# Kernel optimization log

Hardware: AMD Instinct MI355X
Metric: run time of the kernel (lower is better)

The kernel has to match this reference:

```python
import jax, jax.numpy as jnp
import numpy as np

HIDDEN = 8192
K = 32
DIMS = [512, 768]
BATCH = 16384

def _xavier(key, shape):
    fan_out, fan_in = shape
    limit = np.sqrt(6.0 / (fan_in + fan_out)).astype(np.float32)
    return jax.random.uniform(key, shape, dtype=jnp.float32, minval=-limit, maxval=limit)

def setup_inputs() -> dict:
    key = jax.random.key(0)
    ks = jax.random.split(key, 6)
    return {
        "x0": jax.random.normal(ks[0], (BATCH, DIMS[0]), dtype=jnp.float32),
        "x1": jax.random.normal(ks[1], (BATCH, DIMS[1]), dtype=jnp.float32),
        "pre_bias0": jnp.zeros((DIMS[0],), dtype=jnp.float32),
        "pre_bias1": jnp.zeros((DIMS[1],), dtype=jnp.float32),
        "enc_w0": _xavier(ks[2], (HIDDEN, DIMS[0])),   # nn.Linear(d0, hidden).weight
        "enc_w1": _xavier(ks[3], (HIDDEN, DIMS[1])),
        "dec_w0": _xavier(ks[4], (DIMS[0], HIDDEN)),   # nn.Linear(hidden, d0).weight
        "dec_w1": _xavier(ks[5], (DIMS[1], HIDDEN)),
        "post_bias0": jnp.zeros((DIMS[0],), dtype=jnp.float32),
        "post_bias1": jnp.zeros((DIMS[1],), dtype=jnp.float32),
        "source_idx": 0,
    }

def _topk_sparse(z, k):
    # keep top-k per row, zero the rest (hard TopK activation)
    vals, idx = jax.lax.top_k(z, k)                      # [B, k]
    rows = jnp.arange(z.shape[0])[:, None]               # [B, 1]
    return jnp.zeros_like(z).at[rows, idx].set(vals)

def reference(x0, x1, pre_bias0, pre_bias1, enc_w0, enc_w1,
              dec_w0, dec_w1, post_bias0, post_bias1, source_idx):
    xs = (x0, x1)
    pbs = (pre_bias0, pre_bias1)
    ews = (enc_w0, enc_w1)
    # encode from source model: pre-bias subtract -> linear -> TopK sparsify
    x = xs[source_idx]
    z_dense = (x - pbs[source_idx]) @ ews[source_idx].T   # [B, HIDDEN]
    z = _topk_sparse(z_dense, K)
    # decode to every model's activation space
    rec0 = z @ dec_w0.T + post_bias0                      # [B, d0]
    rec1 = z @ dec_w1.T + post_bias1                      # [B, d1]
    return (z, rec0, rec1)
```

## Files before the change

kernel.cpp:

```cpp
#include <hip/hip_runtime.h>


#define BATCH  16384
#define HIDDEN 8192
#define DIM0   512
#define DIM1   768
#define TOPK   32
#define CAND_MAX 256
#define LIST_CAP 128
#define STAGE_CAP 32
#define CNT_STRIDE 16
#define WIN_LO 36
#define WIN_HI 64

#define KLO_G 0xBECDu
#define KHI_G 0xC020u

typedef __attribute__((ext_vector_type(8))) short bf16x8;
typedef __attribute__((ext_vector_type(8))) unsigned short u16x8;
typedef __attribute__((ext_vector_type(4))) float f32x4;

__device__ __forceinline__ unsigned fkey16(unsigned short h) {
    return (h & 0x8000u) ? (unsigned)((~h) & 0xFFFFu) : (unsigned)(h | 0x8000u);
}
__device__ __forceinline__ unsigned short f2b(float f) {
    unsigned u = __float_as_uint(f);
    unsigned r = (u + 0x7FFFu + ((u >> 16) & 1u)) >> 16;
    return (unsigned short)r;
}
__device__ __forceinline__ float b2f(unsigned short h) {
    return __uint_as_float(((unsigned)h) << 16);
}
__device__ __forceinline__ void load_lds16(const void* g, void* l) {
    __builtin_amdgcn_global_load_lds((const __attribute__((address_space(1))) void*)g,
                                     (__attribute__((address_space(3))) void*)l, 16, 0, 0);
}
__device__ __forceinline__ unsigned fkey32(float f) {
    unsigned u = __float_as_uint(f);
    return (u & 0x80000000u) ? ~u : (u | 0x80000000u);
}

__global__ void zero_cnt(int* __restrict__ cnt)
{
    cnt[blockIdx.x * 256 + threadIdx.x] = 0;
}

template<int SRC>
__device__ __forceinline__ void convert_impl(
    const float* __restrict__ x, const float* __restrict__ pb,
    const float* __restrict__ w,
    unsigned short* __restrict__ xb, unsigned short* __restrict__ wb)
{
    constexpr int D = SRC ? DIM1 : DIM0;
    const int nx4 = BATCH * D / 4;
    const int nw4 = HIDDEN * D / 4;
    for (int i = blockIdx.x * blockDim.x + threadIdx.x; i < nx4 + nw4;
         i += gridDim.x * blockDim.x) {
        if (i < nx4) {
            float4 v = ((const float4*)x)[i];
            const int k = (i * 4) % D;
            v.x -= pb[k]; v.y -= pb[k + 1]; v.z -= pb[k + 2]; v.w -= pb[k + 3];
            ushort4 o; o.x = f2b(v.x); o.y = f2b(v.y); o.z = f2b(v.z); o.w = f2b(v.w);
            ((ushort4*)xb)[i] = o;
        } else {
            const float4 v = ((const float4*)w)[i - nx4];
            ushort4 o; o.x = f2b(v.x); o.y = f2b(v.y); o.z = f2b(v.z); o.w = f2b(v.w);
            ((ushort4*)wb)[i - nx4] = o;
        }
    }
}

__global__ void convert_xw(const float* __restrict__ x0, const float* __restrict__ x1,
                           const float* __restrict__ pb0, const float* __restrict__ pb1,
                           const float* __restrict__ w0, const float* __restrict__ w1,
                           const int* __restrict__ srcp,
                           unsigned short* __restrict__ xb, unsigned short* __restrict__ wb)
{
    if (*srcp == 0) convert_impl<0>(x0, pb0, w0, xb, wb);
    else            convert_impl<1>(x1, pb1, w1, xb, wb);
}

__global__ void transpose_dec_bf16(const float* __restrict__ dec,
                                   unsigned short* __restrict__ decT, int DD)
{
    __shared__ float t[32][33];
    const int hb = blockIdx.x * 32, db = blockIdx.y * 32;
    const int lx = threadIdx.x, ly = threadIdx.y;
#pragma unroll
    for (int s = 0; s < 32; s += 8)
        t[ly + s][lx] = dec[(size_t)(db + ly + s) * HIDDEN + hb + lx];
    __syncthreads();
#pragma unroll
    for (int s = 0; s < 32; s += 8)
        decT[(size_t)(hb + ly + s) * DD + db + lx] = f2b(t[lx][ly + s]);
}

template<int SRC>
__device__ __forceinline__ void gemm_impl(
    const unsigned short* __restrict__ xb, const unsigned short* __restrict__ wb,
    float* __restrict__ z, int* __restrict__ cnt, unsigned short* __restrict__ clist,
    unsigned short* As, unsigned short* Bs)
{
    constexpr int D = SRC ? DIM1 : DIM0;
    constexpr unsigned KTH = SRC ? 0xBF86u : 0xBF5Du;

    const int nwg = gridDim.x;
    int id = blockIdx.x;
    id = (id & 7) * (nwg >> 3) + (id >> 3);
    const int bx = id & 63;
    const int by = id >> 6;
    const int m0 = by * 128, n0 = bx * 128;

    const int tid  = threadIdx.x;
    const int lane = tid & 63;
    const int wid  = tid >> 6;
    const int wr   = wid >> 1;
    const int wc   = wid & 1;
    const int l15  = lane & 15;
    const int g    = lane >> 4;

    f32x4 acc[4][4];
#pragma unroll
    for (int i = 0; i < 4; ++i)
#pragma unroll
        for (int j = 0; j < 4; ++j) acc[i][j] = (f32x4){0.f, 0.f, 0.f, 0.f};

    for (int k0 = 0; k0 < D; k0 += 64) {
#pragma unroll
        for (int q = 0; q < 4; ++q) {
            const int c   = wid * 256 + q * 64 + lane;
            const int row = c >> 3, jb = c & 7;
            const int j   = jb ^ (row & 7);
            load_lds16(xb + (size_t)(m0 + row) * D + k0 + j * 8,
                       As + (size_t)(wid * 256 + q * 64) * 8);
            load_lds16(wb + (size_t)(n0 + row) * D + k0 + j * 8,
                       Bs + (size_t)(wid * 256 + q * 64) * 8);
        }
        __syncthreads();

#pragma unroll
        for (int kk = 0; kk < 2; ++kk) {
            bf16x8 a[4], b[4];
#pragma unroll
            for (int f = 0; f < 4; ++f) {
                const int rA = wr * 64 + f * 16 + l15;
                const int sA = ((kk * 4 + g) ^ (rA & 7)) * 16;
                a[f] = *(const bf16x8*)((const char*)As + rA * 128 + sA);
                const int rB = wc * 64 + f * 16 + l15;
                const int sB = ((kk * 4 + g) ^ (rB & 7)) * 16;
                b[f] = *(const bf16x8*)((const char*)Bs + rB * 128 + sB);
            }
#pragma unroll
            for (int fi = 0; fi < 4; ++fi)
#pragma unroll
                for (int fj = 0; fj < 4; ++fj)
                    acc[fi][fj] = __builtin_amdgcn_mfma_f32_16x16x32_bf16(
                        a[fi], b[fj], acc[fi][fj], 0, 0, 0);
        }
        __syncthreads();
    }

    int*            cnt_local = (int*)As;
    int*            base_sh   = (int*)As + 128;
    unsigned short* staging   = (unsigned short*)((int*)As + 256);

    if (tid < 128) cnt_local[tid] = 0;
    __syncthreads();

#pragma unroll
    for (int fi = 0; fi < 4; ++fi) {
        const int rl0 = wr * 64 + fi * 16 + g * 4;
#pragma unroll
        for (int fj = 0; fj < 4; ++fj) {
            const int col = n0 + wc * 64 + fj * 16 + l15;
#pragma unroll
            for (int r = 0; r < 4; ++r) {
                const unsigned short sb = f2b(acc[fi][fj][r]);
                unsigned short* zs =
                    (unsigned short*)((char*)z + (size_t)(m0 + rl0 + r) * (HIDDEN * 4));
                zs[col] = sb;
                if (fkey16(sb) > KTH) {
                    const int ls = atomicAdd(&cnt_local[rl0 + r], 1);
                    if (ls < STAGE_CAP)
                        staging[(rl0 + r) * STAGE_CAP + ls] = (unsigned short)col;
                }
            }
        }
    }
    __syncthreads();

    if (tid < 128) {
        const int n = cnt_local[tid];
        if (n > 0) {
            const int add = (n > STAGE_CAP) ? 1000 : n;
            base_sh[tid] = atomicAdd(&cnt[(size_t)(m0 + tid) * CNT_STRIDE], add);
        }
    }
    __syncthreads();

    if (tid < 128) {
        const int n = min(cnt_local[tid], STAGE_CAP);
        if (n > 0) {
            const int base = base_sh[tid];
            for (int j = 0; j < n; ++j) {
                const int pos = base + j;
                if (pos < LIST_CAP)
                    clist[(size_t)(m0 + tid) * LIST_CAP + pos] =
                        staging[tid * STAGE_CAP + j];
            }
        }
    }

    if (bx >= 32) {
        const f32x4 zv = (f32x4){0.f, 0.f, 0.f, 0.f};
        const int c4 = (4096 >> 2) + (bx - 32) * 32 + (tid & 31);
#pragma unroll
        for (int pass = 0; pass < 16; ++pass) {
            const int r = m0 + pass * 8 + (tid >> 5);
            __builtin_nontemporal_store(zv, (f32x4*)(z + (size_t)r * HIDDEN) + c4);
        }
    }
}

__global__ __launch_bounds__(256, 2)
void gemm_bf16(const unsigned short* __restrict__ xb, const unsigned short* __restrict__ wb,
               const int* __restrict__ srcp, float* __restrict__ z,
               int* __restrict__ cnt, unsigned short* __restrict__ clist)
{
    __shared__ unsigned short As[128 * 64];
    __shared__ unsigned short Bs[128 * 64];
    if (*srcp == 0) gemm_impl<0>(xb, wb, z, cnt, clist, As, Bs);
    else            gemm_impl<1>(xb, wb, z, cnt, clist, As, Bs);
}

template<int SRC>
__device__ __forceinline__ void topk_impl(
    float* __restrict__ z,
    const float* __restrict__ xsrc, const float* __restrict__ pb,
    const float* __restrict__ ew,
    const unsigned short* __restrict__ dTb0, const unsigned short* __restrict__ dTb1,
    const float* __restrict__ po0, const float* __restrict__ po1,
    float* __restrict__ rec0, float* __restrict__ rec1,
    const int* __restrict__ cnt, const unsigned short* __restrict__ clist,
    float* xs, int* cidx, float* cval, unsigned char* cflag,
    int* counts, unsigned* pcounts, int* s_cnt, float* selv, int* seli)
{
    constexpr int D = SRC ? DIM1 : DIM0;

    const int tid = threadIdx.x;
    const size_t row = blockIdx.x;
    float* __restrict__ zrow = z + row * HIDDEN;
    const unsigned short* __restrict__ zsrow =
        (const unsigned short*)((const char*)z + row * (HIDDEN * 4));

    if (tid < D / 4) {
        const float4 xv = ((const float4*)(xsrc + row * D))[tid];
        const float4 pv = ((const float4*)pb)[tid];
        ((float4*)xs)[tid] = make_float4(xv.x - pv.x, xv.y - pv.y,
                                         xv.z - pv.z, xv.w - pv.w);
    }
    if (tid == 0) *s_cnt = 0;

    const int cn = cnt[row * CNT_STRIDE];
    const bool uselist = (cn >= WIN_LO && cn <= LIST_CAP);
    const f32x4 zv4 = (f32x4){0.f, 0.f, 0.f, 0.f};
    int C;

    if (uselist) {
        if (tid < cn) cidx[tid] = (int)clist[row * LIST_CAP + tid];
#pragma unroll
        for (int s = 0; s < 4; ++s)
            __builtin_nontemporal_store(zv4, (f32x4*)&zrow[(size_t)(s * 256 + tid) * 4]);
        __syncthreads();
        C = cn;
    } else {
        unsigned pkey[16];
#pragma unroll
        for (int s = 0; s < 4; ++s) {
            const u16x8 v = *(const u16x8*)(zsrow + (size_t)(s * 256 + tid) * 8);
#pragma unroll
            for (int p = 0; p < 4; ++p)
                pkey[s * 4 + p] = fkey16(v[2 * p]) | (fkey16(v[2 * p + 1]) << 16);
        }
#pragma unroll
        for (int s = 0; s < 4; ++s)
            __builtin_nontemporal_store(zv4, (f32x4*)&zrow[(size_t)(s * 256 + tid) * 4]);

        {
            int clo = 0, chi = 0;
#pragma unroll
            for (int p = 0; p < 16; ++p) {
                const unsigned klo16 = pkey[p] & 0xFFFFu, khi16 = pkey[p] >> 16;
                clo += (klo16 > KLO_G) ? 1 : 0;  chi += (klo16 > KHI_G) ? 1 : 0;
                clo += (khi16 > KLO_G) ? 1 : 0;  chi += (khi16 > KHI_G) ? 1 : 0;
            }
            unsigned pk = (unsigned)clo | ((unsigned)chi << 16);
#pragma unroll
            for (int off = 32; off; off >>= 1) pk += __shfl_xor(pk, off);
            if ((tid & 63) == 0) pcounts[tid >> 6] = pk;
        }
        __syncthreads();
        const unsigned ptot = pcounts[0] + pcounts[1] + pcounts[2] + pcounts[3];
        const int tot_lo = (int)(ptot & 0xFFFFu), tot_hi = (int)(ptot >> 16);

        unsigned kappa;
        int found = 0;
        if (tot_lo >= WIN_LO && tot_lo <= WIN_HI)      { kappa = KLO_G; found = 1; }
        else if (tot_hi >= WIN_LO && tot_hi <= WIN_HI) { kappa = KHI_G; found = 1; }
        if (!found) {
            unsigned lo = 0u, hi = 65535u;
            if (tot_lo > WIN_HI) lo = KLO_G;
            if (tot_lo < WIN_LO) hi = KLO_G;
            if (tot_hi > WIN_HI) lo = KHI_G;
            if (tot_hi < WIN_LO) hi = (hi < KHI_G) ? hi : KHI_G;
            kappa = lo;
            for (int it = 0; it < 18; ++it) {
                const unsigned mid = (lo + hi) >> 1;
                int c = 0;
#pragma unroll
                for (int p = 0; p < 16; ++p) {
                    c += ((pkey[p] & 0xFFFFu) > mid) ? 1 : 0;
                    c += ((pkey[p] >> 16)     > mid) ? 1 : 0;
                }
#pragma unroll
                for (int off = 32; off; off >>= 1) c += __shfl_xor(c, off);
                if ((tid & 63) == 0) counts[(it & 1) * 4 + (tid >> 6)] = c;
                __syncthreads();
                const int* cb = counts + (it & 1) * 4;
                const int tot = cb[0] + cb[1] + cb[2] + cb[3];
                if (tot >= WIN_LO && tot <= WIN_HI) { kappa = mid; break; }
                if (tot > WIN_HI) lo = mid; else hi = mid;
                kappa = lo;
                if (hi - lo <= 1u) break;
            }
        }

#pragma unroll
        for (int p = 0; p < 16; ++p) {
#pragma unroll
            for (int h = 0; h < 2; ++h) {
                const unsigned k16 = h ? (pkey[p] >> 16) : (pkey[p] & 0xFFFFu);
                if (k16 > kappa) {
                    const int j = 2 * p + h;
                    const int slot = atomicAdd(s_cnt, 1);
                    if (slot < CAND_MAX)
                        cidx[slot] = ((j >> 3) * 256 + tid) * 8 + (j & 7);
                }
            }
        }
        __syncthreads();
        C = min(*s_cnt, CAND_MAX);
    }

    {
        constexpr int NB = D / 64;
        const int grp = tid >> 4, j16 = tid & 15;
        for (int c = grp; c < C; c += 16) {
            const float* __restrict__ wrow = ew + (size_t)cidx[c] * D;
            float4 wv[NB];
#pragma unroll
            for (int u = 0; u < NB; ++u)
                wv[u] = *(const float4*)&wrow[(u * 16 + j16) * 4];
            float4 a4 = make_float4(0.f, 0.f, 0.f, 0.f);
#pragma unroll
            for (int u = 0; u < NB; ++u) {
                const float4 x4 = *(const float4*)&xs[(u * 16 + j16) * 4];
                a4.x = fmaf(x4.x, wv[u].x, a4.x);
                a4.y = fmaf(x4.y, wv[u].y, a4.y);
                a4.z = fmaf(x4.z, wv[u].z, a4.z);
                a4.w = fmaf(x4.w, wv[u].w, a4.w);
            }
            float a = (a4.x + a4.y) + (a4.z + a4.w);
            a += __shfl_xor(a, 1);
            a += __shfl_xor(a, 2);
            a += __shfl_xor(a, 4);
            a += __shfl_xor(a, 8);
            if (j16 == 0) cval[c] = a;
        }
    }
    __syncthreads();

    if (tid < C) {
        const float v = cval[tid];
        const int  ix = cidx[tid];
        int rank = 0;
        for (int j = 0; j < C; ++j) {
            const float vj = cval[j];
            rank += (vj > v || (vj == v && cidx[j] < ix)) ? 1 : 0;
        }
        cflag[tid] = (rank < TOPK) ? 1 : 0;
    }
    __syncthreads();
    if (tid < C && cflag[tid]) {
        const int ix = cidx[tid];
        int sr = 0;
        for (int j = 0; j < C; ++j) sr += (cflag[j] && cidx[j] < ix) ? 1 : 0;
        selv[sr] = cval[tid];
        seli[sr] = ix;
    }
    __syncthreads();

    if (tid < TOPK) zrow[seli[tid]] = selv[tid];

#pragma unroll
    for (int pass = 0; pass < 2; ++pass) {
        const int slot = pass * 256 + tid;
        if (slot < (DIM0 + DIM1) / 4) {
            const bool is0 = slot < DIM0 / 4;
            const int d0 = is0 ? slot * 4 : (slot - DIM0 / 4) * 4;
            const int DD = is0 ? DIM0 : DIM1;
            const unsigned short* __restrict__ dT = is0 ? dTb0 : dTb1;
            const float* __restrict__ po = is0 ? po0 : po1;
            f32x4 a;
            {
                const float4 p4 = *(const float4*)&po[d0];
                a = (f32x4){p4.x, p4.y, p4.z, p4.w};
            }
#pragma unroll
            for (int b = 0; b < TOPK / 16; ++b) {
                ushort4 wv[16];
#pragma unroll
                for (int u = 0; u < 16; ++u)
                    wv[u] = *(const ushort4*)&dT[(size_t)seli[b * 16 + u] * DD + d0];
#pragma unroll
                for (int u = 0; u < 16; ++u) {
                    const float sv = selv[b * 16 + u];
                    a.x = fmaf(sv, b2f(wv[u].x), a.x);
                    a.y = fmaf(sv, b2f(wv[u].y), a.y);
                    a.z = fmaf(sv, b2f(wv[u].z), a.z);
                    a.w = fmaf(sv, b2f(wv[u].w), a.w);
                }
            }
            float* __restrict__ out = is0 ? (rec0 + row * DIM0 + d0)
                                          : (rec1 + row * DIM1 + d0);
            __builtin_nontemporal_store(a, (f32x4*)out);
        }
    }
}

__global__ __launch_bounds__(256, 4)
void topk_rescore_decode(float* __restrict__ z,
                         const float* __restrict__ x0, const float* __restrict__ x1,
                         const float* __restrict__ pb0, const float* __restrict__ pb1,
                         const float* __restrict__ ew0, const float* __restrict__ ew1,
                         const unsigned short* __restrict__ dTb0,
                         const unsigned short* __restrict__ dTb1,
                         const float* __restrict__ po0, const float* __restrict__ po1,
                         float* __restrict__ rec0, float* __restrict__ rec1,
                         const int* __restrict__ srcp,
                         const int* __restrict__ cnt, const unsigned short* __restrict__ clist)
{
    __shared__ float         xs[DIM1];
    __shared__ int           cidx[CAND_MAX];
    __shared__ float         cval[CAND_MAX];
    __shared__ unsigned char cflag[CAND_MAX];
    __shared__ int           counts[2 * 4];
    __shared__ unsigned      pcounts[4];
    __shared__ int           s_cnt;
    __shared__ float         selv[TOPK];
    __shared__ int           seli[TOPK];

    if (*srcp == 0)
        topk_impl<0>(z, x0, pb0, ew0, dTb0, dTb1, po0, po1, rec0, rec1, cnt, clist,
                     xs, cidx, cval, cflag, counts, pcounts, &s_cnt, selv, seli);
    else
        topk_impl<1>(z, x1, pb1, ew1, dTb0, dTb1, po0, po1, rec0, rec1, cnt, clist,
                     xs, cidx, cval, cflag, counts, pcounts, &s_cnt, selv, seli);
}


__global__ __launch_bounds__(256, 2)
void encode_gemm(const float* __restrict__ x0, const float* __restrict__ x1,
                 const float* __restrict__ pb0, const float* __restrict__ pb1,
                 const float* __restrict__ w0, const float* __restrict__ w1,
                 const int* __restrict__ srcp, float* __restrict__ z)
{
    const int src = *srcp;
    const float* __restrict__ x  = (src == 0) ? x0 : x1;
    const float* __restrict__ pb = (src == 0) ? pb0 : pb1;
    const float* __restrict__ w  = (src == 0) ? w0 : w1;
    const int D = (src == 0) ? DIM0 : DIM1;

    __shared__ float As[16][132];
    __shared__ float Bs[16][132];

    const int tid = threadIdx.x;
    const int m0 = blockIdx.y * 128;
    const int n0 = blockIdx.x * 128;

    const int cA0 = tid,          cA1 = tid + 256;
    const int r0  = cA0 >> 2,     kq0 = (cA0 & 3) * 4;
    const int r1  = cA1 >> 2,     kq1 = (cA1 & 3) * 4;

    const int mf = (tid & 15) * 4;
    const int nf = (tid >> 4) * 4;

    float acc[8][8];
#pragma unroll
    for (int i = 0; i < 8; ++i)
#pragma unroll
        for (int j = 0; j < 8; ++j) acc[i][j] = 0.0f;

    for (int k0 = 0; k0 < D; k0 += 16) {
        const float4 av0 = *(const float4*)(x + (size_t)(m0 + r0) * D + k0 + kq0);
        const float4 av1 = *(const float4*)(x + (size_t)(m0 + r1) * D + k0 + kq1);
        const float4 pv0 = *(const float4*)(pb + k0 + kq0);
        const float4 pv1 = *(const float4*)(pb + k0 + kq1);
        const float4 bv0 = *(const float4*)(w + (size_t)(n0 + r0) * D + k0 + kq0);
        const float4 bv1 = *(const float4*)(w + (size_t)(n0 + r1) * D + k0 + kq1);
        As[kq0 + 0][r0] = av0.x - pv0.x;
        As[kq0 + 1][r0] = av0.y - pv0.y;
        As[kq0 + 2][r0] = av0.z - pv0.z;
        As[kq0 + 3][r0] = av0.w - pv0.w;
        As[kq1 + 0][r1] = av1.x - pv1.x;
        As[kq1 + 1][r1] = av1.y - pv1.y;
        As[kq1 + 2][r1] = av1.z - pv1.z;
        As[kq1 + 3][r1] = av1.w - pv1.w;
        Bs[kq0 + 0][r0] = bv0.x;
        Bs[kq0 + 1][r0] = bv0.y;
        Bs[kq0 + 2][r0] = bv0.z;
        Bs[kq0 + 3][r0] = bv0.w;
        Bs[kq1 + 0][r1] = bv1.x;
        Bs[kq1 + 1][r1] = bv1.y;
        Bs[kq1 + 2][r1] = bv1.z;
        Bs[kq1 + 3][r1] = bv1.w;
        __syncthreads();
#pragma unroll
        for (int kk = 0; kk < 16; ++kk) {
            const float4 A0 = *(const float4*)&As[kk][mf];
            const float4 A1 = *(const float4*)&As[kk][mf + 64];
            const float4 B0 = *(const float4*)&Bs[kk][nf];
            const float4 B1 = *(const float4*)&Bs[kk][nf + 64];
            const float a[8] = {A0.x, A0.y, A0.z, A0.w, A1.x, A1.y, A1.z, A1.w};
            const float b[8] = {B0.x, B0.y, B0.z, B0.w, B1.x, B1.y, B1.z, B1.w};
#pragma unroll
            for (int i = 0; i < 8; ++i)
#pragma unroll
                for (int j = 0; j < 8; ++j)
                    acc[i][j] = fmaf(a[i], b[j], acc[i][j]);
        }
        __syncthreads();
    }

#pragma unroll
    for (int i = 0; i < 8; ++i) {
        const int row = m0 + mf + (i & 3) + (i >> 2) * 64;
        const float4 v0 = make_float4(acc[i][0], acc[i][1], acc[i][2], acc[i][3]);
        const float4 v1 = make_float4(acc[i][4], acc[i][5], acc[i][6], acc[i][7]);
        *(float4*)(z + (size_t)row * HIDDEN + n0 + nf)      = v0;
        *(float4*)(z + (size_t)row * HIDDEN + n0 + nf + 64) = v1;
    }
}

__global__ __launch_bounds__(256, 2)
void topk_decode_fb(float* __restrict__ z,
                    const float* __restrict__ dA, const float* __restrict__ dB,
                    const float* __restrict__ po0, const float* __restrict__ po1,
                    float* __restrict__ rec0, float* __restrict__ rec1)
{
    __shared__ float    rowv[HIDDEN];
    __shared__ unsigned hist[4][257];
    __shared__ unsigned scanbuf[256];
    __shared__ float    selv[TOPK];
    __shared__ int      seli[TOPK];
    __shared__ unsigned sh_byte, sh_gt;

    const int tid = threadIdx.x;
    const size_t rowid = blockIdx.x;
    float* __restrict__ zrow = z + rowid * HIDDEN;

#pragma unroll
    for (int s = 0; s < 8; ++s) {
        const int i4 = s * 256 + tid;
        *(float4*)&rowv[i4 * 4] = *(const float4*)&zrow[i4 * 4];
    }
    __syncthreads();

    unsigned prefix = 0, prefmask = 0, need = TOPK;
#pragma unroll
    for (int p = 3; p >= 0; --p) {
        for (int i = tid; i < 4 * 257; i += 256) (&hist[0][0])[i] = 0;
        __syncthreads();
        const int sh = p * 8;
        for (int s = 0; s < 32; ++s) {
            const int i = s * 256 + tid;
            const unsigned k = fkey32(rowv[i]);
            if ((k & prefmask) == prefix)
                atomicAdd(&hist[tid & 3][(k >> sh) & 255], 1);
        }
        __syncthreads();
        const unsigned tot = hist[0][tid] + hist[1][tid] + hist[2][tid] + hist[3][tid];
        hist[0][tid] = tot;
        __syncthreads();
        if (tid == 0) {
            unsigned cum = 0;
            int b = 255;
            for (;; --b) {
                const unsigned c = hist[0][b];
                if (cum + c >= need || b == 0) { sh_byte = (unsigned)b; sh_gt = cum; break; }
                cum += c;
            }
        }
        __syncthreads();
        prefix  |= sh_byte << sh;
        prefmask |= 0xFFu << sh;
        need -= sh_gt;
        __syncthreads();
    }
    const unsigned cut = prefix;
    const unsigned needEq = need;

    unsigned gtmask = 0, eqmask = 0;
#pragma unroll
    for (int j = 0; j < 32; ++j) {
        const int jr = (j + tid) & 31;
        const int i = tid * 32 + jr;
        const unsigned k = fkey32(rowv[i]);
        if (k > cut)       gtmask |= 1u << jr;
        else if (k == cut) eqmask |= 1u << jr;
    }

    scanbuf[tid] = __popc(eqmask);
    __syncthreads();
    for (int off = 1; off < 256; off <<= 1) {
        const unsigned v = scanbuf[tid];
        const unsigned add = (tid >= off) ? scanbuf[tid - off] : 0u;
        __syncthreads();
        scanbuf[tid] = v + add;
        __syncthreads();
    }
    const unsigned eqexc = scanbuf[tid] - __popc(eqmask);
    __syncthreads();

    unsigned selmask = gtmask;
    {
        unsigned m = eqmask, r = eqexc;
        while (m) {
            const int j = __ffs(m) - 1;
            if (r < needEq) selmask |= 1u << j;
            ++r;
            m &= m - 1;
        }
    }

    scanbuf[tid] = __popc(selmask);
    __syncthreads();
    for (int off = 1; off < 256; off <<= 1) {
        const unsigned v = scanbuf[tid];
        const unsigned add = (tid >= off) ? scanbuf[tid - off] : 0u;
        __syncthreads();
        scanbuf[tid] = v + add;
        __syncthreads();
    }
    const unsigned selexc = scanbuf[tid] - __popc(selmask);

#pragma unroll
    for (int j = 0; j < 32; ++j) {
        const int jr = (j + tid) & 31;
        const int i = tid * 32 + jr;
        if ((selmask >> jr) & 1u) {
            const int slot = (int)(selexc + __popc(selmask & ((1u << jr) - 1u)));
            selv[slot] = rowv[i];
            seli[slot] = i;
        } else {
            rowv[i] = 0.0f;
        }
    }
    __syncthreads();

#pragma unroll
    for (int s = 0; s < 8; ++s) {
        const int i4 = s * 256 + tid;
        *(float4*)&zrow[i4 * 4] = *(float4*)&rowv[i4 * 4];
    }

    for (int d = tid; d < DIM0; d += 256) {
        float a = po0[d];
#pragma unroll
        for (int j = 0; j < TOPK; ++j)
            a = fmaf(selv[j], dA[(size_t)d * HIDDEN + seli[j]], a);
        rec0[rowid * DIM0 + d] = a;
    }
    for (int d = tid; d < DIM1; d += 256) {
        float a = po1[d];
#pragma unroll
        for (int j = 0; j < TOPK; ++j)
            a = fmaf(selv[j], dB[(size_t)d * HIDDEN + seli[j]], a);
        rec1[rowid * DIM1 + d] = a;
    }
}

extern "C" void kernel_launch(void* const* d_in, const int* in_sizes, int n_in,
                              void* d_out, int out_size, void* d_ws, size_t ws_size,
                              hipStream_t stream)
{
    const float* x0  = (const float*)d_in[0];
    const float* x1  = (const float*)d_in[1];
    const float* pb0 = (const float*)d_in[2];
    const float* pb1 = (const float*)d_in[3];
    const float* ew0 = (const float*)d_in[4];
    const float* ew1 = (const float*)d_in[5];
    const float* dw0 = (const float*)d_in[6];
    const float* dw1 = (const float*)d_in[7];
    const float* po0 = (const float*)d_in[8];
    const float* po1 = (const float*)d_in[9];
    const int*  srcp = (const int*)d_in[10];

    float* z    = (float*)d_out;
    float* rec0 = z + (size_t)BATCH * HIDDEN;
    float* rec1 = rec0 + (size_t)BATCH * DIM0;

    unsigned short* xb   = (unsigned short*)d_ws;
    unsigned short* wb   = xb   + (size_t)BATCH * DIM1;
    unsigned short* dTb0 = wb   + (size_t)HIDDEN * DIM1;
    unsigned short* dTb1 = dTb0 + (size_t)HIDDEN * DIM0;
    int*            cnt  = (int*)(dTb1 + (size_t)HIDDEN * DIM1);
    unsigned short* clist = (unsigned short*)(cnt + (size_t)BATCH * CNT_STRIDE);
    const size_t need = ((size_t)BATCH * DIM1 + (size_t)HIDDEN * DIM1 +
                         (size_t)HIDDEN * DIM0 + (size_t)HIDDEN * DIM1) * sizeof(unsigned short)
                        + (size_t)BATCH * CNT_STRIDE * sizeof(int)
                        + (size_t)BATCH * LIST_CAP * sizeof(unsigned short);

    if (ws_size >= need) {
        zero_cnt<<<(BATCH * CNT_STRIDE) / 256, 256, 0, stream>>>(cnt);
        convert_xw<<<4096, 256, 0, stream>>>(x0, x1, pb0, pb1, ew0, ew1, srcp, xb, wb);
        dim3 tb(32, 8);
        transpose_dec_bf16<<<dim3(HIDDEN / 32, DIM0 / 32), tb, 0, stream>>>(dw0, dTb0, DIM0);
        transpose_dec_bf16<<<dim3(HIDDEN / 32, DIM1 / 32), tb, 0, stream>>>(dw1, dTb1, DIM1);
        gemm_bf16<<<(BATCH / 128) * (HIDDEN / 128), 256, 0, stream>>>(
            xb, wb, srcp, z, cnt, clist);
        topk_rescore_decode<<<BATCH, 256, 0, stream>>>(
            z, x0, x1, pb0, pb1, ew0, ew1, dTb0, dTb1, po0, po1, rec0, rec1,
            srcp, cnt, clist);
    } else {
        encode_gemm<<<dim3(HIDDEN / 128, BATCH / 128), 256, 0, stream>>>(
            x0, x1, pb0, pb1, ew0, ew1, srcp, z);
        topk_decode_fb<<<BATCH, 256, 0, stream>>>(z, dw0, dw1, po0, po1, rec0, rec1);
    }
}
```

Baseline: 688.5 us.

## Drop bf16 z staging, rescore only top candidates, add exact fallback kernel

The GEMM epilogue no longer writes bf16 scores into z. It now zeros the whole z tile and stages candidate entries as packed (key, column) words chosen by a float threshold. The top-k kernel ranks list candidates and rescores only the best 40 in fp32, and returns early for rows whose candidate count falls outside the window. A new fixup kernel recomputes the full fp32 row with a radix select for those rows. This removes bf16 z traffic and the per-row histogram/bisection path, at the cost of an extra launch and a slow scalar path for outlier rows. It also risks missing true top-k elements when fewer than 40 rescored candidates hold them.

```diff
diff --git a/kernel.cpp b/kernel.cpp
--- a/kernel.cpp
+++ b/kernel.cpp
@@ -6,18 +6,13 @@
 #define DIM0   512
 #define DIM1   768
 #define TOPK   32
-#define CAND_MAX 256
 #define LIST_CAP 128
+#define RESCORE_TOP 40
 #define STAGE_CAP 32
 #define CNT_STRIDE 16
 #define WIN_LO 36
-#define WIN_HI 64
-
-#define KLO_G 0xBECDu
-#define KHI_G 0xC020u
 
 typedef __attribute__((ext_vector_type(8))) short bf16x8;
-typedef __attribute__((ext_vector_type(8))) unsigned short u16x8;
 typedef __attribute__((ext_vector_type(4))) float f32x4;
 
 __device__ __forceinline__ unsigned fkey16(unsigned short h) {
@@ -98,11 +93,11 @@
 template<int SRC>
 __device__ __forceinline__ void gemm_impl(
     const unsigned short* __restrict__ xb, const unsigned short* __restrict__ wb,
-    float* __restrict__ z, int* __restrict__ cnt, unsigned short* __restrict__ clist,
+    float* __restrict__ z, int* __restrict__ cnt, unsigned* __restrict__ clist,
     unsigned short* As, unsigned short* Bs)
 {
     constexpr int D = SRC ? DIM1 : DIM0;
-    constexpr unsigned KTH = SRC ? 0xBF86u : 0xBF5Du;
+    constexpr float THETA = SRC ? 0.96761f : 0.80161f;
 
     const int nwg = gridDim.x;
     int id = blockIdx.x;
@@ -160,9 +155,9 @@
         __syncthreads();
     }
 
-    int*            cnt_local = (int*)As;
-    int*            base_sh   = (int*)As + 128;
-    unsigned short* staging   = (unsigned short*)((int*)As + 256);
+    unsigned* staging   = (unsigned*)As;
+    int*      cnt_local = (int*)Bs;
+    int*      base_sh   = (int*)Bs + 128;
 
     if (tid < 128) cnt_local[tid] = 0;
     __syncthreads();
@@ -175,14 +170,12 @@
             const int col = n0 + wc * 64 + fj * 16 + l15;
 #pragma unroll
             for (int r = 0; r < 4; ++r) {
-                const unsigned short sb = f2b(acc[fi][fj][r]);
-                unsigned short* zs =
-                    (unsigned short*)((char*)z + (size_t)(m0 + rl0 + r) * (HIDDEN * 4));
-                zs[col] = sb;
-                if (fkey16(sb) > KTH) {
+                const float v = acc[fi][fj][r];
+                if (v > THETA) {
                     const int ls = atomicAdd(&cnt_local[rl0 + r], 1);
                     if (ls < STAGE_CAP)
-                        staging[(rl0 + r) * STAGE_CAP + ls] = (unsigned short)col;
+                        staging[(rl0 + r) * STAGE_CAP + ls] =
+                            (fkey16(f2b(v)) << 16) | (0xFFFFu - (unsigned)col);
                 }
             }
         }
@@ -211,9 +204,9 @@
         }
     }
 
-    if (bx >= 32) {
+    {
         const f32x4 zv = (f32x4){0.f, 0.f, 0.f, 0.f};
-        const int c4 = (4096 >> 2) + (bx - 32) * 32 + (tid & 31);
+        const int c4 = bx * 32 + (tid & 31);
 #pragma unroll
         for (int pass = 0; pass < 16; ++pass) {
             const int r = m0 + pass * 8 + (tid >> 5);
@@ -225,7 +218,7 @@
 __global__ __launch_bounds__(256, 2)
 void gemm_bf16(const unsigned short* __restrict__ xb, const unsigned short* __restrict__ wb,
                const int* __restrict__ srcp, float* __restrict__ z,
-               int* __restrict__ cnt, unsigned short* __restrict__ clist)
+               int* __restrict__ cnt, unsigned* __restrict__ clist)
 {
     __shared__ unsigned short As[128 * 64];
     __shared__ unsigned short Bs[128 * 64];
@@ -241,17 +234,18 @@
     const unsigned short* __restrict__ dTb0, const unsigned short* __restrict__ dTb1,
     const float* __restrict__ po0, const float* __restrict__ po1,
     float* __restrict__ rec0, float* __restrict__ rec1,
-    const int* __restrict__ cnt, const unsigned short* __restrict__ clist,
-    float* xs, int* cidx, float* cval, unsigned char* cflag,
-    int* counts, unsigned* pcounts, int* s_cnt, float* selv, int* seli)
+    const int* __restrict__ cnt, const unsigned* __restrict__ clist,
+    float* xs, unsigned* centry, int* cidx, float* cval, unsigned char* cflag,
+    float* selv, int* seli)
 {
     constexpr int D = SRC ? DIM1 : DIM0;
 
     const int tid = threadIdx.x;
     const size_t row = blockIdx.x;
     float* __restrict__ zrow = z + row * HIDDEN;
-    const unsigned short* __restrict__ zsrow =
-        (const unsigned short*)((const char*)z + row * (HIDDEN * 4));
+
+    const int cn = cnt[row * CNT_STRIDE];
+    if (cn < WIN_LO || cn > LIST_CAP) return;
 
     if (tid < D / 4) {
         const float4 xv = ((const float4*)(xsrc + row * D))[tid];
@@ -259,98 +253,17 @@
         ((float4*)xs)[tid] = make_float4(xv.x - pv.x, xv.y - pv.y,
                                          xv.z - pv.z, xv.w - pv.w);
     }
-    if (tid == 0) *s_cnt = 0;
-
-    const int cn = cnt[row * CNT_STRIDE];
-    const bool uselist = (cn >= WIN_LO && cn <= LIST_CAP);
-    const f32x4 zv4 = (f32x4){0.f, 0.f, 0.f, 0.f};
-    int C;
-
-    if (uselist) {
-        if (tid < cn) cidx[tid] = (int)clist[row * LIST_CAP + tid];
-#pragma unroll
-        for (int s = 0; s < 4; ++s)
-            __builtin_nontemporal_store(zv4, (f32x4*)&zrow[(size_t)(s * 256 + tid) * 4]);
-        __syncthreads();
-        C = cn;
-    } else {
-        unsigned pkey[16];
-#pragma unroll
-        for (int s = 0; s < 4; ++s) {
-            const u16x8 v = *(const u16x8*)(zsrow + (size_t)(s * 256 + tid) * 8);
-#pragma unroll
-            for (int p = 0; p < 4; ++p)
-                pkey[s * 4 + p] = fkey16(v[2 * p]) | (fkey16(v[2 * p + 1]) << 16);
-        }
-#pragma unroll
-        for (int s = 0; s < 4; ++s)
-            __builtin_nontemporal_store(zv4, (f32x4*)&zrow[(size_t)(s * 256 + tid) * 4]);
-
-        {
-            int clo = 0, chi = 0;
-#pragma unroll
-            for (int p = 0; p < 16; ++p) {
-                const unsigned klo16 = pkey[p] & 0xFFFFu, khi16 = pkey[p] >> 16;
-                clo += (klo16 > KLO_G) ? 1 : 0;  chi += (klo16 > KHI_G) ? 1 : 0;
-                clo += (khi16 > KLO_G) ? 1 : 0;  chi += (khi16 > KHI_G) ? 1 : 0;
-            }
-            unsigned pk = (unsigned)clo | ((unsigned)chi << 16);
-#pragma unroll
-            for (int off = 32; off; off >>= 1) pk += __shfl_xor(pk, off);
-            if ((tid & 63) == 0) pcounts[tid >> 6] = pk;
-        }
-        __syncthreads();
-        const unsigned ptot = pcounts[0] + pcounts[1] + pcounts[2] + pcounts[3];
-        const int tot_lo = (int)(ptot & 0xFFFFu), tot_hi = (int)(ptot >> 16);
-
-        unsigned kappa;
-        int found = 0;
-        if (tot_lo >= WIN_LO && tot_lo <= WIN_HI)      { kappa = KLO_G; found = 1; }
-        else if (tot_hi >= WIN_LO && tot_hi <= WIN_HI) { kappa = KHI_G; found = 1; }
-        if (!found) {
-            unsigned lo = 0u, hi = 65535u;
-            if (tot_lo > WIN_HI) lo = KLO_G;
-            if (tot_lo < WIN_LO) hi = KLO_G;
-            if (tot_hi > WIN_HI) lo = KHI_G;
-            if (tot_hi < WIN_LO) hi = (hi < KHI_G) ? hi : KHI_G;
-            kappa = lo;
-            for (int it = 0; it < 18; ++it) {
-                const unsigned mid = (lo + hi) >> 1;
-                int c = 0;
-#pragma unroll
-                for (int p = 0; p < 16; ++p) {
-                    c += ((pkey[p] & 0xFFFFu) > mid) ? 1 : 0;
-                    c += ((pkey[p] >> 16)     > mid) ? 1 : 0;
-                }
-#pragma unroll
-                for (int off = 32; off; off >>= 1) c += __shfl_xor(c, off);
-                if ((tid & 63) == 0) counts[(it & 1) * 4 + (tid >> 6)] = c;
-                __syncthreads();
-                const int* cb = counts + (it & 1) * 4;
-                const int tot = cb[0] + cb[1] + cb[2] + cb[3];
-                if (tot >= WIN_LO && tot <= WIN_HI) { kappa = mid; break; }
-                if (tot > WIN_HI) lo = mid; else hi = mid;
-                kappa = lo;
-                if (hi - lo <= 1u) break;
-            }
-        }
-
-#pragma unroll
-        for (int p = 0; p < 16; ++p) {
-#pragma unroll
-            for (int h = 0; h < 2; ++h) {
-                const unsigned k16 = h ? (pkey[p] >> 16) : (pkey[p] & 0xFFFFu);
-                if (k16 > kappa) {
-                    const int j = 2 * p + h;
-                    const int slot = atomicAdd(s_cnt, 1);
-                    if (slot < CAND_MAX)
-                        cidx[slot] = ((j >> 3) * 256 + tid) * 8 + (j & 7);
-                }
-            }
-        }
-        __syncthreads();
-        C = min(*s_cnt, CAND_MAX);
-    }
+    if (tid < cn) centry[tid] = clist[row * LIST_CAP + tid];
+    __syncthreads();
+
+    const int C = min(cn, RESCORE_TOP);
+    if (tid < cn) {
+        const unsigned e = centry[tid];
+        int rank = 0;
+        for (int j = 0; j < cn; ++j) rank += (centry[j] > e) ? 1 : 0;
+        if (rank < RESCORE_TOP) cidx[rank] = (int)(0xFFFFu - (e & 0xFFFFu));
+    }
+    __syncthreads();
 
     {
         constexpr int NB = D / 64;
@@ -448,24 +361,220 @@
                          const float* __restrict__ po0, const float* __restrict__ po1,
                          float* __restrict__ rec0, float* __restrict__ rec1,
                          const int* __restrict__ srcp,
-                         const int* __restrict__ cnt, const unsigned short* __restrict__ clist)
+                         const int* __restrict__ cnt, const unsigned* __restrict__ clist)
 {
     __shared__ float         xs[DIM1];
-    __shared__ int           cidx[CAND_MAX];
-    __shared__ float         cval[CAND_MAX];
-    __shared__ unsigned char cflag[CAND_MAX];
-    __shared__ int           counts[2 * 4];
-    __shared__ unsigned      pcounts[4];
-    __shared__ int           s_cnt;
+    __shared__ unsigned      centry[LIST_CAP];
+    __shared__ int           cidx[RESCORE_TOP];
+    __shared__ float         cval[RESCORE_TOP];
+    __shared__ unsigned char cflag[RESCORE_TOP];
     __shared__ float         selv[TOPK];
     __shared__ int           seli[TOPK];
 
     if (*srcp == 0)
         topk_impl<0>(z, x0, pb0, ew0, dTb0, dTb1, po0, po1, rec0, rec1, cnt, clist,
-                     xs, cidx, cval, cflag, counts, pcounts, &s_cnt, selv, seli);
+                     xs, centry, cidx, cval, cflag, selv, seli);
     else
         topk_impl<1>(z, x1, pb1, ew1, dTb0, dTb1, po0, po1, rec0, rec1, cnt, clist,
-                     xs, cidx, cval, cflag, counts, pcounts, &s_cnt, selv, seli);
+                     xs, centry, cidx, cval, cflag, selv, seli);
+}
+
+template<int SRC>
+__device__ __forceinline__ void fixup_impl(
+    float* __restrict__ z,
+    const float* __restrict__ xsrc, const float* __restrict__ pb,
+    const float* __restrict__ ew,
+    const unsigned short* __restrict__ dTb0, const unsigned short* __restrict__ dTb1,
+    const float* __restrict__ po0, const float* __restrict__ po1,
+    float* __restrict__ rec0, float* __restrict__ rec1,
+    float* sc, float* xs, unsigned* hist, unsigned* scanbuf,
+    float* selv, int* seli, unsigned* sh2)
+{
+    constexpr int D = SRC ? DIM1 : DIM0;
+    const int tid = threadIdx.x;
+    const size_t row = blockIdx.x;
+    float* __restrict__ zrow = z + row * HIDDEN;
+
+    if (tid < D / 4) {
+        const float4 xv = ((const float4*)(xsrc + row * D))[tid];
+        const float4 pv = ((const float4*)pb)[tid];
+        ((float4*)xs)[tid] = make_float4(xv.x - pv.x, xv.y - pv.y,
+                                         xv.z - pv.z, xv.w - pv.w);
+    }
+    __syncthreads();
+
+    for (int s = 0; s < 32; ++s) {
+        const int c = s * 256 + tid;
+        const float* __restrict__ wrow = ew + (size_t)c * D;
+        float a = 0.0f;
+        for (int k = 0; k < D; k += 4) {
+            const float4 w4 = *(const float4*)&wrow[k];
+            a = fmaf(xs[k + 0], w4.x, a);
+            a = fmaf(xs[k + 1], w4.y, a);
+            a = fmaf(xs[k + 2], w4.z, a);
+            a = fmaf(xs[k + 3], w4.w, a);
+        }
+        sc[c] = a;
+    }
+    __syncthreads();
+
+    unsigned prefix = 0, prefmask = 0, need = TOPK;
+#pragma unroll
+    for (int p = 3; p >= 0; --p) {
+        for (int i = tid; i < 4 * 257; i += 256) hist[i] = 0;
+        __syncthreads();
+        const int sh = p * 8;
+        for (int s = 0; s < 32; ++s) {
+            const int i = s * 256 + tid;
+            const unsigned k = fkey32(sc[i]);
+            if ((k & prefmask) == prefix)
+                atomicAdd(&hist[(tid & 3) * 257 + ((k >> sh) & 255)], 1);
+        }
+        __syncthreads();
+        const unsigned tot = hist[0 * 257 + tid] + hist[1 * 257 + tid] +
+                             hist[2 * 257 + tid] + hist[3 * 257 + tid];
+        hist[tid] = tot;
+        __syncthreads();
+        if (tid == 0) {
+            unsigned cum = 0;
+            int b = 255;
+            for (;; --b) {
+                const unsigned c = hist[b];
+                if (cum + c >= need || b == 0) { sh2[0] = (unsigned)b; sh2[1] = cum; break; }
+                cum += c;
+            }
+        }
+        __syncthreads();
+        prefix  |= sh2[0] << sh;
+        prefmask |= 0xFFu << sh;
+        need -= sh2[1];
+        __syncthreads();
+    }
+    const unsigned cut = prefix;
+    const unsigned needEq = need;
+
+    unsigned gtmask = 0, eqmask = 0;
+#pragma unroll
+    for (int j = 0; j < 32; ++j) {
+        const int jr = (j + tid) & 31;
+        const int i = tid * 32 + jr;
+        const unsigned k = fkey32(sc[i]);
+        if (k > cut)       gtmask |= 1u << jr;
+        else if (k == cut) eqmask |= 1u << jr;
+    }
+
+    scanbuf[tid] = __popc(eqmask);
+    __syncthreads();
+    for (int off = 1; off < 256; off <<= 1) {
+        const unsigned v = scanbuf[tid];
+        const unsigned add = (tid >= off) ? scanbuf[tid - off] : 0u;
+        __syncthreads();
+        scanbuf[tid] = v + add;
+        __syncthreads();
+    }
+    const unsigned eqexc = scanbuf[tid] - __popc(eqmask);
+    __syncthreads();
+
+    unsigned selmask = gtmask;
+    {
+        unsigned m = eqmask, r = eqexc;
+        while (m) {
+            const int j = __ffs(m) - 1;
+            if (r < needEq) selmask |= 1u << j;
+            ++r;
+            m &= m - 1;
+        }
+    }
+
+    scanbuf[tid] = __popc(selmask);
+    __syncthreads();
+    for (int off = 1; off < 256; off <<= 1) {
+        const unsigned v = scanbuf[tid];
+        const unsigned add = (tid >= off) ? scanbuf[tid - off] : 0u;
+        __syncthreads();
+        scanbuf[tid] = v + add;
+        __syncthreads();
+    }
+    const unsigned selexc = scanbuf[tid] - __popc(selmask);
+
+#pragma unroll
+    for (int j = 0; j < 32; ++j) {
+        const int jr = (j + tid) & 31;
+        const int i = tid * 32 + jr;
+        if ((selmask >> jr) & 1u) {
+            const int slot = (int)(selexc + __popc(selmask & ((1u << jr) - 1u)));
+            selv[slot] = sc[i];
+            seli[slot] = i;
+        }
+    }
+    __syncthreads();
+
+    if (tid < TOPK) zrow[seli[tid]] = selv[tid];
+
+#pragma unroll
+    for (int pass = 0; pass < 2; ++pass) {
+        const int slot = pass * 256 + tid;
+        if (slot < (DIM0 + DIM1) / 4) {
+            const bool is0 = slot < DIM0 / 4;
+            const int d0 = is0 ? slot * 4 : (slot - DIM0 / 4) * 4;
+            const int DD = is0 ? DIM0 : DIM1;
+            const unsigned short* __restrict__ dT = is0 ? dTb0 : dTb1;
+            const float* __restrict__ po = is0 ? po0 : po1;
+            f32x4 a;
+            {
+                const float4 p4 = *(const float4*)&po[d0];
+                a = (f32x4){p4.x, p4.y, p4.z, p4.w};
+            }
+#pragma unroll
+            for (int b = 0; b < TOPK / 16; ++b) {
+                ushort4 wv[16];
+#pragma unroll
+                for (int u = 0; u < 16; ++u)
+                    wv[u] = *(const ushort4*)&dT[(size_t)seli[b * 16 + u] * DD + d0];
+#pragma unroll
+                for (int u = 0; u < 16; ++u) {
+                    const float sv = selv[b * 16 + u];
+                    a.x = fmaf(sv, b2f(wv[u].x), a.x);
+                    a.y = fmaf(sv, b2f(wv[u].y), a.y);
+                    a.z = fmaf(sv, b2f(wv[u].z), a.z);
+                    a.w = fmaf(sv, b2f(wv[u].w), a.w);
+                }
+            }
+            float* __restrict__ out = is0 ? (rec0 + row * DIM0 + d0)
+                                          : (rec1 + row * DIM1 + d0);
+            __builtin_nontemporal_store(a, (f32x4*)out);
+        }
+    }
+}
+
+__global__ __launch_bounds__(256)
+void fixup_topk(float* __restrict__ z,
+                const float* __restrict__ x0, const float* __restrict__ x1,
+                const float* __restrict__ pb0, const float* __restrict__ pb1,
+                const float* __restrict__ ew0, const float* __restrict__ ew1,
+                const unsigned short* __restrict__ dTb0,
+                const unsigned short* __restrict__ dTb1,
+                const float* __restrict__ po0, const float* __restrict__ po1,
+                float* __restrict__ rec0, float* __restrict__ rec1,
+                const int* __restrict__ srcp, const int* __restrict__ cnt)
+{
+    const int cn = cnt[(size_t)blockIdx.x * CNT_STRIDE];
+    if (cn >= WIN_LO && cn <= LIST_CAP) return;
+
+    __shared__ float    sc[HIDDEN];
+    __shared__ float    xs[DIM1];
+    __shared__ unsigned hist[4 * 257];
+    __shared__ unsigned scanbuf[256];
+    __shared__ float    selv[TOPK];
+    __shared__ int      seli[TOPK];
+    __shared__ unsigned sh2[2];
+
+    if (*srcp == 0)
+        fixup_impl<0>(z, x0, pb0, ew0, dTb0, dTb1, po0, po1, rec0, rec1,
+                      sc, xs, hist, scanbuf, selv, seli, sh2);
+    else
+        fixup_impl<1>(z, x1, pb1, ew1, dTb0, dTb1, po0, po1, rec0, rec1,
+                      sc, xs, hist, scanbuf, selv, seli, sh2);
 }
 
 
@@ -715,11 +824,11 @@
     unsigned short* dTb0 = wb   + (size_t)HIDDEN * DIM1;
     unsigned short* dTb1 = dTb0 + (size_t)HIDDEN * DIM0;
     int*            cnt  = (int*)(dTb1 + (size_t)HIDDEN * DIM1);
-    unsigned short* clist = (unsigned short*)(cnt + (size_t)BATCH * CNT_STRIDE);
+    unsigned*       clist = (unsigned*)(cnt + (size_t)BATCH * CNT_STRIDE);
     const size_t need = ((size_t)BATCH * DIM1 + (size_t)HIDDEN * DIM1 +
                          (size_t)HIDDEN * DIM0 + (size_t)HIDDEN * DIM1) * sizeof(unsigned short)
                         + (size_t)BATCH * CNT_STRIDE * sizeof(int)
-                        + (size_t)BATCH * LIST_CAP * sizeof(unsigned short);
+                        + (size_t)BATCH * LIST_CAP * sizeof(unsigned);
 
     if (ws_size >= need) {
         zero_cnt<<<(BATCH * CNT_STRIDE) / 256, 256, 0, stream>>>(cnt);
@@ -732,6 +841,9 @@
         topk_rescore_decode<<<BATCH, 256, 0, stream>>>(
             z, x0, x1, pb0, pb1, ew0, ew1, dTb0, dTb1, po0, po1, rec0, rec1,
             srcp, cnt, clist);
+        fixup_topk<<<BATCH, 256, 0, stream>>>(
+            z, x0, x1, pb0, pb1, ew0, ew1, dTb0, dTb1, po0, po1, rec0, rec1,
+            srcp, cnt);
     } else {
         encode_gemm<<<dim3(HIDDEN / 128, BATCH / 128), 256, 0, stream>>>(
             x0, x1, pb0, pb1, ew0, ew1, srcp, z);
```

Measured after the change: 1.533 ms. 2.23x slower.

## Rank bf16 candidates and rescore only the top 40 in fp32

Applied to the files above, without the earlier changes.

Candidate entries now pack the bf16 sort key with the column index, both in the GEMM staging list and in the top-k kernel's fallback path. The top-k kernel ranks the candidates by that key and rescores only the best RESCORE_TOP=40 in exact fp32, instead of all of them (up to 128 or 256). This is meant to cut the per-row fp32 recompute work. In exchange the candidate list doubles in size (32-bit entries), a quadratic rank pass is added, and results can be wrong if a true top-32 element ranks below 40th under bf16 rounding.

```diff
diff --git a/kernel.cpp b/kernel.cpp
--- a/kernel.cpp
+++ b/kernel.cpp
@@ -8,6 +8,7 @@
 #define TOPK   32
 #define CAND_MAX 256
 #define LIST_CAP 128
+#define RESCORE_TOP 40
 #define STAGE_CAP 32
 #define CNT_STRIDE 16
 #define WIN_LO 36
@@ -98,7 +99,7 @@
 template<int SRC>
 __device__ __forceinline__ void gemm_impl(
     const unsigned short* __restrict__ xb, const unsigned short* __restrict__ wb,
-    float* __restrict__ z, int* __restrict__ cnt, unsigned short* __restrict__ clist,
+    float* __restrict__ z, int* __restrict__ cnt, unsigned* __restrict__ clist,
     unsigned short* As, unsigned short* Bs)
 {
     constexpr int D = SRC ? DIM1 : DIM0;
@@ -160,9 +161,9 @@
         __syncthreads();
     }
 
-    int*            cnt_local = (int*)As;
-    int*            base_sh   = (int*)As + 128;
-    unsigned short* staging   = (unsigned short*)((int*)As + 256);
+    unsigned* staging   = (unsigned*)As;
+    int*      cnt_local = (int*)Bs;
+    int*      base_sh   = (int*)Bs + 128;
 
     if (tid < 128) cnt_local[tid] = 0;
     __syncthreads();
@@ -179,10 +180,12 @@
                 unsigned short* zs =
                     (unsigned short*)((char*)z + (size_t)(m0 + rl0 + r) * (HIDDEN * 4));
                 zs[col] = sb;
-                if (fkey16(sb) > KTH) {
+                const unsigned k16 = fkey16(sb);
+                if (k16 > KTH) {
                     const int ls = atomicAdd(&cnt_local[rl0 + r], 1);
                     if (ls < STAGE_CAP)
-                        staging[(rl0 + r) * STAGE_CAP + ls] = (unsigned short)col;
+                        staging[(rl0 + r) * STAGE_CAP + ls] =
+                            (k16 << 16) | (unsigned)(8191 - col);
                 }
             }
         }
@@ -225,7 +228,7 @@
 __global__ __launch_bounds__(256, 2)
 void gemm_bf16(const unsigned short* __restrict__ xb, const unsigned short* __restrict__ wb,
                const int* __restrict__ srcp, float* __restrict__ z,
-               int* __restrict__ cnt, unsigned short* __restrict__ clist)
+               int* __restrict__ cnt, unsigned* __restrict__ clist)
 {
     __shared__ unsigned short As[128 * 64];
     __shared__ unsigned short Bs[128 * 64];
@@ -241,8 +244,8 @@
     const unsigned short* __restrict__ dTb0, const unsigned short* __restrict__ dTb1,
     const float* __restrict__ po0, const float* __restrict__ po1,
     float* __restrict__ rec0, float* __restrict__ rec1,
-    const int* __restrict__ cnt, const unsigned short* __restrict__ clist,
-    float* xs, int* cidx, float* cval, unsigned char* cflag,
+    const int* __restrict__ cnt, const unsigned* __restrict__ clist,
+    float* xs, unsigned* centry, int* cidx, float* cval, unsigned char* cflag,
     int* counts, unsigned* pcounts, int* s_cnt, float* selv, int* seli)
 {
     constexpr int D = SRC ? DIM1 : DIM0;
@@ -264,15 +267,15 @@
     const int cn = cnt[row * CNT_STRIDE];
     const bool uselist = (cn >= WIN_LO && cn <= LIST_CAP);
     const f32x4 zv4 = (f32x4){0.f, 0.f, 0.f, 0.f};
-    int C;
+    int cnC;
 
     if (uselist) {
-        if (tid < cn) cidx[tid] = (int)clist[row * LIST_CAP + tid];
+        if (tid < cn) centry[tid] = clist[row * LIST_CAP + tid];
 #pragma unroll
         for (int s = 0; s < 4; ++s)
             __builtin_nontemporal_store(zv4, (f32x4*)&zrow[(size_t)(s * 256 + tid) * 4]);
         __syncthreads();
-        C = cn;
+        cnC = cn;
     } else {
         unsigned pkey[16];
 #pragma unroll
@@ -343,14 +346,25 @@
                 if (k16 > kappa) {
                     const int j = 2 * p + h;
                     const int slot = atomicAdd(s_cnt, 1);
-                    if (slot < CAND_MAX)
-                        cidx[slot] = ((j >> 3) * 256 + tid) * 8 + (j & 7);
+                    if (slot < CAND_MAX) {
+                        const int idx = ((j >> 3) * 256 + tid) * 8 + (j & 7);
+                        centry[slot] = (k16 << 16) | (unsigned)(8191 - idx);
+                    }
                 }
             }
         }
         __syncthreads();
-        C = min(*s_cnt, CAND_MAX);
-    }
+        cnC = min(*s_cnt, CAND_MAX);
+    }
+
+    const int C = min(cnC, RESCORE_TOP);
+    if (tid < cnC) {
+        const unsigned e = centry[tid];
+        int rank = 0;
+        for (int j = 0; j < cnC; ++j) rank += (centry[j] > e) ? 1 : 0;
+        if (rank < RESCORE_TOP) cidx[rank] = 8191 - (int)(e & 0xFFFFu);
+    }
+    __syncthreads();
 
     {
         constexpr int NB = D / 64;
@@ -448,12 +462,13 @@
                          const float* __restrict__ po0, const float* __restrict__ po1,
                          float* __restrict__ rec0, float* __restrict__ rec1,
                          const int* __restrict__ srcp,
-                         const int* __restrict__ cnt, const unsigned short* __restrict__ clist)
+                         const int* __restrict__ cnt, const unsigned* __restrict__ clist)
 {
     __shared__ float         xs[DIM1];
-    __shared__ int           cidx[CAND_MAX];
-    __shared__ float         cval[CAND_MAX];
-    __shared__ unsigned char cflag[CAND_MAX];
+    __shared__ unsigned      centry[CAND_MAX];
+    __shared__ int           cidx[RESCORE_TOP];
+    __shared__ float         cval[RESCORE_TOP];
+    __shared__ unsigned char cflag[RESCORE_TOP];
     __shared__ int           counts[2 * 4];
     __shared__ unsigned      pcounts[4];
     __shared__ int           s_cnt;
@@ -462,10 +477,10 @@
 
     if (*srcp == 0)
         topk_impl<0>(z, x0, pb0, ew0, dTb0, dTb1, po0, po1, rec0, rec1, cnt, clist,
-                     xs, cidx, cval, cflag, counts, pcounts, &s_cnt, selv, seli);
+                     xs, centry, cidx, cval, cflag, counts, pcounts, &s_cnt, selv, seli);
     else
         topk_impl<1>(z, x1, pb1, ew1, dTb0, dTb1, po0, po1, rec0, rec1, cnt, clist,
-                     xs, cidx, cval, cflag, counts, pcounts, &s_cnt, selv, seli);
+                     xs, centry, cidx, cval, cflag, counts, pcounts, &s_cnt, selv, seli);
 }
 
 
@@ -715,11 +730,11 @@
     unsigned short* dTb0 = wb   + (size_t)HIDDEN * DIM1;
     unsigned short* dTb1 = dTb0 + (size_t)HIDDEN * DIM0;
     int*            cnt  = (int*)(dTb1 + (size_t)HIDDEN * DIM1);
-    unsigned short* clist = (unsigned short*)(cnt + (size_t)BATCH * CNT_STRIDE);
+    unsigned*       clist = (unsigned*)(cnt + (size_t)BATCH * CNT_STRIDE);
     const size_t need = ((size_t)BATCH * DIM1 + (size_t)HIDDEN * DIM1 +
                          (size_t)HIDDEN * DIM0 + (size_t)HIDDEN * DIM1) * sizeof(unsigned short)
                         + (size_t)BATCH * CNT_STRIDE * sizeof(int)
-                        + (size_t)BATCH * LIST_CAP * sizeof(unsigned short);
+                        + (size_t)BATCH * LIST_CAP * sizeof(unsigned);
 
     if (ws_size >= need) {
         zero_cnt<<<(BATCH * CNT_STRIDE) / 256, 256, 0, stream>>>(cnt);
```

Measured after the change: 640.3 us, median of 2. -7.0%, faster.
